# Optimization experiments

Hardware: AMD Instinct MI355X
Metric: run time of the kernel (lower is better)

## Reference

```python
import jax, jax.numpy as jnp
import numpy as np

B, T, N, E = 4, 30, 2000, 32000
F_IN, F_HID, F_GRU, N_CLS = 8, 64, 128, 2


def setup_inputs() -> dict:
    key = jax.random.key(0)
    ks = jax.random.split(key, 12)
    return {
        "x": jax.random.normal(ks[0], (B, T, N, F_IN), jnp.float32),
        "edge_index": jax.random.randint(ks[1], (B, T, 2, E), 0, N, jnp.int32),
        "W1": jax.random.normal(ks[2], (F_IN, F_HID), jnp.float32) * 0.1,
        "b1": jax.random.normal(ks[3], (F_HID,), jnp.float32) * 0.1,
        "W2": jax.random.normal(ks[4], (F_HID, F_HID), jnp.float32) * 0.1,
        "b2": jax.random.normal(ks[5], (F_HID,), jnp.float32) * 0.1,
        "W_ih": jax.random.normal(ks[6], (3 * F_GRU, F_HID), jnp.float32) * 0.1,
        "W_hh": jax.random.normal(ks[7], (3 * F_GRU, F_GRU), jnp.float32) * 0.1,
        "b_ih": jax.random.normal(ks[8], (3 * F_GRU,), jnp.float32) * 0.1,
        "b_hh": jax.random.normal(ks[9], (3 * F_GRU,), jnp.float32) * 0.1,
        "fc_w": jax.random.normal(ks[10], (N_CLS, F_GRU), jnp.float32) * 0.1,
        "fc_b": jax.random.normal(ks[11], (N_CLS,), jnp.float32) * 0.1,
    }


def _gcn_conv(x, src, dst, W, b):
    # PyG GCNConv (edge_weight=None): add self-loops, sym-normalize, x@W, scatter-add, +bias
    n = x.shape[0]
    loops = jnp.arange(n, dtype=src.dtype)
    s = jnp.concatenate([src, loops])
    d = jnp.concatenate([dst, loops])
    deg = jax.ops.segment_sum(jnp.ones(s.shape[0], x.dtype), d, num_segments=n)
    dis = jnp.where(deg > 0, jax.lax.rsqrt(deg), 0.0)
    norm = dis[s] * dis[d]                      # [E+N]
    h = x @ W                                   # [N, Fout]
    msg = h[s] * norm[:, None]                  # gather + scale
    return jax.ops.segment_sum(msg, d, num_segments=n) + b


def _frame_embed(x, ei, W1, b1, W2, b2):
    # one graph frame -> mean-pooled 64-d embedding
    src, dst = ei[0], ei[1]
    h = jax.nn.relu(_gcn_conv(x, src, dst, W1, b1))
    h = jax.nn.relu(_gcn_conv(h, src, dst, W2, b2))
    return h.mean(axis=0)


def _gru(H, W_ih, W_hh, b_ih, b_hh):
    # H: [T, B, F_HID]; torch GRU gate order: r, z, n
    def step(h, x_t):
        gi = x_t @ W_ih.T + b_ih                # [B, 3H]
        gh = h @ W_hh.T + b_hh
        i_r, i_z, i_n = jnp.split(gi, 3, axis=-1)
        h_r, h_z, h_n = jnp.split(gh, 3, axis=-1)
        r = jax.nn.sigmoid(i_r + h_r)
        z = jax.nn.sigmoid(i_z + h_z)
        n = jnp.tanh(i_n + r * h_n)
        h_new = (1.0 - z) * n + z * h
        return h_new, None
    h0 = jnp.zeros((H.shape[1], F_GRU), H.dtype)
    h_final, _ = jax.lax.scan(step, h0, H)
    return h_final                              # [B, F_GRU]


def reference(x, edge_index, W1, b1, W2, b2, W_ih, W_hh, b_ih, b_hh, fc_w, fc_b):
    G = B * T
    xf = x.reshape(G, N, F_IN)
    eif = edge_index.reshape(G, 2, E)
    emb = jax.vmap(_frame_embed, in_axes=(0, 0, None, None, None, None))(
        xf, eif, W1, b1, W2, b2)                # [G, 64]
    H = emb.reshape(B, T, F_HID).transpose(1, 0, 2)  # [T, B, 64]
    h_final = _gru(H, W_ih, W_hh, b_ih, b_hh)   # [B, 128]
    return h_final @ fc_w.T + fc_b              # [B, 2]
```

## Files before the change

kernel.cpp:

```cpp
#include <hip/hip_runtime.h>
#include <math.h>

#define G    120
#define Nn   2000
#define Ee   32000
#define Tt   30
#define Bb   4
#define Fg   128
#define QCAP 9216
#define TSLOT 48

static __device__ __forceinline__ unsigned short f2bf(float f) {
    unsigned u = __float_as_uint(f);
    u += 0x7fffu + ((u >> 16) & 1u);
    return (unsigned short)(u >> 16);
}

#if defined(__has_builtin)
#if __has_builtin(__builtin_amdgcn_cvt_f32_fp8) && __has_builtin(__builtin_amdgcn_cvt_pk_fp8_f32)
#define HW_FP8 1
#endif
#if __has_builtin(__builtin_amdgcn_cvt_pk_f32_fp8)
#define HW_FP8_PK 1
typedef float floatx2 __attribute__((ext_vector_type(2)));
#endif
#endif

static __device__ __forceinline__ unsigned fp8_enc_sw(float x) {
    unsigned s = (__float_as_uint(x) >> 24) & 0x80u;
    float ax = fminf(fabsf(x), 448.f);
    unsigned em;
    if (ax < 0.015625f) {
        em = (unsigned)__float2int_rn(ax * 512.f);
    } else {
        int e = (int)(__float_as_uint(ax) >> 23) - 127;
        float r = ax * __uint_as_float((unsigned)((130 - e) << 23));
        int q = __float2int_rn(r);
        em = (unsigned)(((e + 7) << 3) + (q - 8));
        em = min(em, 126u);
    }
    return s | em;
}
static __device__ __forceinline__ float fp8_dec_sw(unsigned b) {
    unsigned em = b & 0x7fu;
    float mag;
    if (em < 8u) mag = (float)em * 0.001953125f;
    else mag = __uint_as_float((((em >> 3) + 120u) << 23) | ((em & 7u) << 20));
    return (b & 0x80u) ? -mag : mag;
}
static __device__ __forceinline__ unsigned fp8_pack4(float a, float b, float c, float d) {
#ifdef HW_FP8
    int w = __builtin_amdgcn_cvt_pk_fp8_f32(a, b, 0, false);
    w = __builtin_amdgcn_cvt_pk_fp8_f32(c, d, w, true);
    return (unsigned)w;
#else
    return fp8_enc_sw(a) | (fp8_enc_sw(b) << 8) | (fp8_enc_sw(c) << 16) | (fp8_enc_sw(d) << 24);
#endif
}
static __device__ __forceinline__ void fp8x4_dec(unsigned dw, float* o) {
#ifdef HW_FP8_PK
    floatx2 lo = __builtin_amdgcn_cvt_pk_f32_fp8((int)dw, false);
    floatx2 hi = __builtin_amdgcn_cvt_pk_f32_fp8((int)dw, true);
    o[0] = lo[0]; o[1] = lo[1]; o[2] = hi[0]; o[3] = hi[1];
#else
    o[0] = fp8_dec_sw(dw & 0xffu);
    o[1] = fp8_dec_sw((dw >> 8) & 0xffu);
    o[2] = fp8_dec_sw((dw >> 16) & 0xffu);
    o[3] = fp8_dec_sw((dw >> 24) & 0xffu);
#endif
}

__global__ void __launch_bounds__(1024, 1)
k_build(const int* __restrict__ ei, float* __restrict__ dis,
        int* __restrict__ startA, int* __restrict__ csr,
        unsigned* __restrict__ ellT, int* __restrict__ cntS,
        int* __restrict__ ordS, float* __restrict__ emb) {
    __shared__ int   csr_l[Ee];
    __shared__ int   hist[Nn];
    __shared__ int   cntL[Nn];
    __shared__ int   nodeAt[Nn];
    __shared__ float disl[Nn];
    __shared__ int   dh[64];
    __shared__ int   db[64];
    __shared__ int   ovfS;
    int g = blockIdx.x;
    int tid = threadIdx.x;
    for (int idx = tid; idx < Nn; idx += 1024) hist[idx] = 0;
    if (tid < 64) dh[tid] = 0;
    if (tid == 0) ovfS = 0;
    if (tid < 64) emb[g * 64 + tid] = 0.f;
    __syncthreads();
    const int* srcp = ei + (size_t)g * 2 * Ee;
    const int* dstp = srcp + Ee;
    for (int it = tid; it < Ee / 4; it += 1024) {
        int4 d = reinterpret_cast<const int4*>(dstp)[it];
        atomicAdd(&hist[d.x], 1);
        atomicAdd(&hist[d.y], 1);
        atomicAdd(&hist[d.z], 1);
        atomicAdd(&hist[d.w], 1);
    }
    __syncthreads();
    for (int idx = tid; idx < Nn; idx += 1024) {
        int c = hist[idx];
        cntL[idx] = c;
        float dv = rsqrtf((float)c + 1.0f);
        disl[idx] = dv;
        dis[(size_t)g * Nn + idx] = dv;
        atomicAdd(&dh[min(c, 63)], 1);
        if (c > TSLOT - 1) atomicMax(&ovfS, 1);
    }
    __syncthreads();
    for (int off = 1; off < Nn; off <<= 1) {
        int i1 = tid + 1024;
        int v0 = (tid >= off) ? hist[tid - off] : 0;
        int v1 = (i1 < Nn && i1 >= off) ? hist[i1 - off] : 0;
        __syncthreads();
        hist[tid] += v0;
        if (i1 < Nn) hist[i1] += v1;
        __syncthreads();
    }
    if (tid == 0) {
        int s = 0;
        for (int b = 0; b < 64; ++b) { db[b] = s; s += dh[b]; }
    }
    __syncthreads();
    if (tid < 64) dh[tid] = db[tid];
    __syncthreads();
    for (int idx = tid; idx < Nn; idx += 1024) {
        int p = atomicAdd(&dh[min(cntL[idx], 63)], 1);
        nodeAt[p] = idx;
        hist[idx] -= cntL[idx];
    }
    __syncthreads();
    for (int it = tid; it < Ee / 4; it += 1024) {
        int4 d = reinterpret_cast<const int4*>(dstp)[it];
        int4 s = reinterpret_cast<const int4*>(srcp)[it];
        csr_l[atomicAdd(&hist[d.x], 1)] = s.x;
        csr_l[atomicAdd(&hist[d.y], 1)] = s.y;
        csr_l[atomicAdd(&hist[d.z], 1)] = s.z;
        csr_l[atomicAdd(&hist[d.w], 1)] = s.w;
    }
    __syncthreads();
    for (int c = tid; c < Nn; c += 1024) {
        int n2 = nodeAt[c];
        int cnt2 = cntL[n2];
        int ex2 = hist[n2] - cnt2;
        size_t gc = (size_t)g * Nn + c;
        cntS[gc] = cnt2;
        ordS[gc] = n2;
        startA[(size_t)g * Nn + n2] = g * 4 * QCAP + ex2;
        float dn2 = disl[n2];
        unsigned* et = ellT + (size_t)g * TSLOT * Nn + c;
        et[0] = (unsigned)n2 | ((unsigned)f2bf(dn2 * dn2) << 16);
        int m2 = min(cnt2, TSLOT - 1);
        for (int e = 0; e < m2; ++e) {
            int s = csr_l[ex2 + e];
            et[(size_t)(e + 1) * Nn] = (unsigned)s | ((unsigned)f2bf(disl[s] * dn2) << 16);
        }
    }
    __syncthreads();
    if (ovfS) {
        int* cg = csr + (size_t)g * 4 * QCAP;
        for (int it = tid; it < Ee; it += 1024) cg[it] = csr_l[it];
    }
}

__global__ void __launch_bounds__(256)
k_fused(const float* __restrict__ x, const unsigned* __restrict__ ellT,
        const int* __restrict__ cntS, const int* __restrict__ ordS,
        const int* __restrict__ startA, const int* __restrict__ csr,
        const float* __restrict__ dis,
        const float* __restrict__ W1, const float* __restrict__ b1,
        const float* __restrict__ W2, unsigned char* __restrict__ t2f) {
    int i = blockIdx.x;
    int xcd = i & 7;
    int j = i >> 3;
    int g = xcd * 15 + (j >> 3);
    int blk = j & 7;
    int p = blk * 256 + threadIdx.x;
    bool valid = (p < Nn);
    size_t gp = (size_t)g * Nn + (valid ? p : 0);
    int n = valid ? ordS[gp] : 0;
    int cnt = valid ? cntS[gp] : 0;
    int myc = valid ? (min(cnt, TSLOT - 1) + 1) : 0;
    float aX[8];
#pragma unroll
    for (int k = 0; k < 8; ++k) aX[k] = 0.f;
    {
        const unsigned* et = ellT + (size_t)g * TSLOT * Nn + (valid ? p : 0);
        const float4* x4 = reinterpret_cast<const float4*>(x + (size_t)g * Nn * 8);
        for (int e0 = 0; e0 < TSLOT; e0 += 8) {
            if (!__any(e0 < myc)) break;
            unsigned ub[8];
#pragma unroll
            for (int k = 0; k < 8; ++k)
                ub[k] = (e0 + k < myc) ? et[(size_t)(e0 + k) * Nn] : 0u;
#pragma unroll
            for (int k = 0; k < 8; ++k) {
                if (e0 + k < myc) {
                    float w = __uint_as_float(ub[k] & 0xffff0000u);
                    int s = ub[k] & 0xffffu;
                    float4 r0 = x4[s * 2], r1 = x4[s * 2 + 1];
                    aX[0] += r0.x * w; aX[1] += r0.y * w; aX[2] += r0.z * w; aX[3] += r0.w * w;
                    aX[4] += r1.x * w; aX[5] += r1.y * w; aX[6] += r1.z * w; aX[7] += r1.w * w;
                }
            }
        }
        if (cnt > TSLOT - 1) {
            size_t gn = (size_t)g * Nn + n;
            float dn = dis[gn];
            int start = startA[gn];
            const float* dsg = dis + (size_t)g * Nn;
            for (int e = TSLOT - 1; e < cnt; ++e) {
                int s = csr[start + e];
                float w = dsg[s] * dn;
                float4 r0 = x4[s * 2], r1 = x4[s * 2 + 1];
                aX[0] += r0.x * w; aX[1] += r0.y * w; aX[2] += r0.z * w; aX[3] += r0.w * w;
                aX[4] += r1.x * w; aX[5] += r1.y * w; aX[6] += r1.z * w; aX[7] += r1.w * w;
            }
        }
    }
    float h1r[64];
    {
        const float4* b14 = reinterpret_cast<const float4*>(b1);
#pragma unroll
        for (int f4 = 0; f4 < 16; ++f4) {
            float4 b = b14[f4];
            h1r[4 * f4 + 0] = b.x; h1r[4 * f4 + 1] = b.y;
            h1r[4 * f4 + 2] = b.z; h1r[4 * f4 + 3] = b.w;
        }
        const float4* W14 = reinterpret_cast<const float4*>(W1);
#pragma unroll
        for (int k = 0; k < 8; ++k) {
            float hk = aX[k];
#pragma unroll
            for (int f4 = 0; f4 < 16; ++f4) {
                float4 w = W14[k * 16 + f4];
                h1r[4 * f4 + 0] += hk * w.x; h1r[4 * f4 + 1] += hk * w.y;
                h1r[4 * f4 + 2] += hk * w.z; h1r[4 * f4 + 3] += hk * w.w;
            }
        }
#pragma unroll
        for (int f = 0; f < 64; ++f) h1r[f] = fmaxf(h1r[f], 0.f);
    }
    uint4 oh[2][2];
    {
        const float4* W24 = reinterpret_cast<const float4*>(W2);
#pragma unroll
        for (int hf = 0; hf < 2; ++hf) {
            float acch[32];
#pragma unroll
            for (int f = 0; f < 32; ++f) acch[f] = 0.f;
#pragma unroll
            for (int k = 0; k < 64; ++k) {
                float hk = h1r[k];
#pragma unroll
                for (int f4 = 0; f4 < 8; ++f4) {
                    float4 w = W24[k * 16 + hf * 8 + f4];
                    acch[4 * f4 + 0] += hk * w.x; acch[4 * f4 + 1] += hk * w.y;
                    acch[4 * f4 + 2] += hk * w.z; acch[4 * f4 + 3] += hk * w.w;
                }
            }
            oh[hf][0].x = fp8_pack4(acch[0],  acch[1],  acch[2],  acch[3]);
            oh[hf][0].y = fp8_pack4(acch[4],  acch[5],  acch[6],  acch[7]);
            oh[hf][0].z = fp8_pack4(acch[8],  acch[9],  acch[10], acch[11]);
            oh[hf][0].w = fp8_pack4(acch[12], acch[13], acch[14], acch[15]);
            oh[hf][1].x = fp8_pack4(acch[16], acch[17], acch[18], acch[19]);
            oh[hf][1].y = fp8_pack4(acch[20], acch[21], acch[22], acch[23]);
            oh[hf][1].z = fp8_pack4(acch[24], acch[25], acch[26], acch[27]);
            oh[hf][1].w = fp8_pack4(acch[28], acch[29], acch[30], acch[31]);
        }
    }
    if (valid) {
        uint4* op = reinterpret_cast<uint4*>(t2f + ((size_t)g * Nn + n) * 64);
        op[0] = oh[0][0]; op[1] = oh[0][1]; op[2] = oh[1][0]; op[3] = oh[1][1];
    }
}

__global__ void __launch_bounds__(1024, 1)
k_aggF(const unsigned char* __restrict__ t2f, const unsigned* __restrict__ ellT,
       const int* __restrict__ cntS, const int* __restrict__ ordS,
       const int* __restrict__ startA, const int* __restrict__ csr,
       const float* __restrict__ dis, const float* __restrict__ bias,
       float* __restrict__ emb) {
    __shared__ uint4 stage[Nn * 5];
    int i = blockIdx.x;
    int xcd = i & 7;
    int j = i >> 3;
    int g = xcd * 15 + (j >> 1);
    int half = j & 1;
    int tid = threadIdx.x;
    int w = tid >> 6, lane = tid & 63;
    {
        const uint4* src = reinterpret_cast<const uint4*>(t2f + (size_t)g * Nn * 64);
        for (int it = tid; it < Nn * 4; it += 1024)
            stage[(it >> 2) * 5 + (it & 3)] = src[it];
    }
    __syncthreads();
#define ROWFMA(dw, base) { float o_[4]; fp8x4_dec(dw, o_); \
    acc[base + 0] += o_[0] * wt; acc[base + 1] += o_[1] * wt; \
    acc[base + 2] += o_[2] * wt; acc[base + 3] += o_[3] * wt; }
#define EDGEFMA(s, wt) { \
    uint4 r0 = stage[(s) * 5], r1 = stage[(s) * 5 + 1]; \
    uint4 r2 = stage[(s) * 5 + 2], r3 = stage[(s) * 5 + 3]; \
    ROWFMA(r0.x, 0)  ROWFMA(r0.y, 4)  ROWFMA(r0.z, 8)  ROWFMA(r0.w, 12) \
    ROWFMA(r1.x, 16) ROWFMA(r1.y, 20) ROWFMA(r1.z, 24) ROWFMA(r1.w, 28) \
    ROWFMA(r2.x, 32) ROWFMA(r2.y, 36) ROWFMA(r2.z, 40) ROWFMA(r2.w, 44) \
    ROWFMA(r3.x, 48) ROWFMA(r3.y, 52) ROWFMA(r3.z, 56) ROWFMA(r3.w, 60) }
    int po = w * 64 + lane;
    int p = half * 1000 + po;
    bool valid = (po < 1000);
    size_t gp = (size_t)g * Nn + (valid ? p : 0);
    int cnt = valid ? cntS[gp] : 0;
    int myc = valid ? (min(cnt, TSLOT - 1) + 1) : 0;
    float acc[64];
#pragma unroll
    for (int k = 0; k < 64; ++k) acc[k] = 0.f;
    const unsigned* et = ellT + (size_t)g * TSLOT * Nn + (valid ? p : 0);
    unsigned u_cur = (0 < myc) ? et[0] : 0u;
    for (int e = 0; e < TSLOT; ++e) {
        if (!__any(e < myc)) break;
        unsigned u_nxt = ((e + 1) < TSLOT && (e + 1) < myc)
                             ? et[(size_t)(e + 1) * Nn] : 0u;
        if (e < myc) {
            float wt = __uint_as_float(u_cur & 0xffff0000u);
            int s = u_cur & 0xffffu;
            EDGEFMA(s, wt)
        }
        u_cur = u_nxt;
    }
    if (cnt > TSLOT - 1) {
        int n = ordS[gp];
        size_t gn = (size_t)g * Nn + n;
        float dn = dis[gn];
        int start = startA[gn];
        const float* dsg = dis + (size_t)g * Nn;
        for (int e = TSLOT - 1; e < cnt; ++e) {
            int s = csr[start + e];
            float wt = dsg[s] * dn;
            EDGEFMA(s, wt)
        }
    }
#undef EDGEFMA
#undef ROWFMA
    float pool = 0.f;
#pragma unroll
    for (int k = 0; k < 64; ++k) {
        float v = valid ? fmaxf(acc[k] + bias[k], 0.f) : 0.f;
        v += __shfl_xor(v, 1);  v += __shfl_xor(v, 2);  v += __shfl_xor(v, 4);
        v += __shfl_xor(v, 8);  v += __shfl_xor(v, 16); v += __shfl_xor(v, 32);
        if (lane == k) pool = v;
    }
    atomicAdd(&emb[g * 64 + lane], pool * (1.0f / Nn));
}

__global__ void __launch_bounds__(768, 1)
k_gru_seq(const float* __restrict__ emb, const float* __restrict__ W_ih,
          const float* __restrict__ b_ih, const float* __restrict__ W_hh,
          const float* __restrict__ b_hh, const float* __restrict__ fc_w,
          const float* __restrict__ fc_b, float* __restrict__ out) {
    __shared__ float h[Fg];
    __shared__ float part[768];
    __shared__ float embs[Tt][64];
    __shared__ float pgi[Tt][768];
    int b = blockIdx.x;
    int tid = threadIdx.x;
    int row = tid >> 1;
    int half = tid & 1;
    float w[64];
    const float* wr = W_hh + (size_t)row * Fg + half * 64;
#pragma unroll
    for (int i = 0; i < 64; ++i) w[i] = wr[i];
    float wih[32];
    const float* wir = W_ih + (size_t)row * 64 + half * 32;
#pragma unroll
    for (int i = 0; i < 32; ++i) wih[i] = wir[i];
    for (int it = tid; it < Tt * 64; it += 768)
        embs[it >> 6][it & 63] = emb[((size_t)b * Tt) * 64 + it];
    if (tid < Fg) h[tid] = 0.f;
    __syncthreads();
    for (int t = 0; t < Tt; ++t) {
        const float* e = &embs[t][half * 32];
        float a0 = 0.f, a1 = 0.f, a2 = 0.f, a3 = 0.f;
#pragma unroll
        for (int i = 0; i < 8; ++i) {
            a0 += wih[4 * i + 0] * e[4 * i + 0];
            a1 += wih[4 * i + 1] * e[4 * i + 1];
            a2 += wih[4 * i + 2] * e[4 * i + 2];
            a3 += wih[4 * i + 3] * e[4 * i + 3];
        }
        pgi[t][tid] = (a0 + a1) + (a2 + a3);
    }
    __syncthreads();
    for (int t = 0; t < Tt; ++t) {
        const float* hh = &h[half * 64];
        float a0 = 0.f, a1 = 0.f, a2 = 0.f, a3 = 0.f;
#pragma unroll
        for (int i = 0; i < 16; ++i) {
            a0 += w[4 * i + 0] * hh[4 * i + 0];
            a1 += w[4 * i + 1] * hh[4 * i + 1];
            a2 += w[4 * i + 2] * hh[4 * i + 2];
            a3 += w[4 * i + 3] * hh[4 * i + 3];
        }
        part[tid] = (a0 + a1) + (a2 + a3);
        __syncthreads();
        if (tid < Fg) {
            int j = tid;
            float hr = b_hh[j]       + part[2 * j]           + part[2 * j + 1];
            float hz = b_hh[128 + j] + part[2 * (128 + j)]   + part[2 * (128 + j) + 1];
            float hn = b_hh[256 + j] + part[2 * (256 + j)]   + part[2 * (256 + j) + 1];
            float gr = b_ih[j]       + pgi[t][2 * j]         + pgi[t][2 * j + 1];
            float gz = b_ih[128 + j] + pgi[t][2 * (128 + j)] + pgi[t][2 * (128 + j) + 1];
            float gn = b_ih[256 + j] + pgi[t][2 * (256 + j)] + pgi[t][2 * (256 + j) + 1];
            float r  = 1.f / (1.f + expf(-(gr + hr)));
            float z  = 1.f / (1.f + expf(-(gz + hz)));
            float nn = tanhf(gn + r * hn);
            h[j] = (1.f - z) * nn + z * h[j];
        }
        __syncthreads();
    }
    if (tid < 2) {
        float acc = fc_b[tid];
        for (int k = 0; k < Fg; ++k) acc += fc_w[tid * Fg + k] * h[k];
        out[b * 2 + tid] = acc;
    }
}

extern "C" void kernel_launch(void* const* d_in, const int* in_sizes, int n_in,
                              void* d_out, int out_size, void* d_ws, size_t ws_size,
                              hipStream_t stream) {
    const float* x     = (const float*)d_in[0];
    const int*   ei    = (const int*)  d_in[1];
    const float* W1    = (const float*)d_in[2];
    const float* b1    = (const float*)d_in[3];
    const float* W2    = (const float*)d_in[4];
    const float* b2    = (const float*)d_in[5];
    const float* W_ih  = (const float*)d_in[6];
    const float* W_hh  = (const float*)d_in[7];
    const float* b_ih  = (const float*)d_in[8];
    const float* b_hh  = (const float*)d_in[9];
    const float* fc_w  = (const float*)d_in[10];
    const float* fc_b  = (const float*)d_in[11];
    float* out = (float*)d_out;

    char* ws = (char*)d_ws;
    size_t off = 0;
    auto alloc = [&](size_t bytes) -> void* {
        void* p = ws + off;
        off = (off + bytes + 255) & ~(size_t)255;
        return p;
    };
    float*    dis    = (float*)   alloc((size_t)G * Nn * 4);
    int*      startA = (int*)     alloc((size_t)G * Nn * 4);
    int*      cntS   = (int*)     alloc((size_t)G * Nn * 4);
    int*      ordS   = (int*)     alloc((size_t)G * Nn * 4);
    int*      csr    = (int*)     alloc((size_t)G * 4 * QCAP * 4);
    unsigned* ellT   = (unsigned*)alloc((size_t)G * TSLOT * Nn * 4);
    unsigned char* t2f = (unsigned char*)alloc((size_t)G * Nn * 64);
    float*    emb    = (float*)   alloc((size_t)G * 64 * 4);
    (void)ws_size; (void)in_sizes; (void)n_in; (void)out_size;

    hipLaunchKernelGGL(k_build,   dim3(G), dim3(1024), 0, stream, ei, dis, startA, csr, ellT, cntS, ordS, emb);
    hipLaunchKernelGGL(k_fused,   dim3(960), dim3(256), 0, stream, x, ellT, cntS, ordS, startA, csr, dis, W1, b1, W2, t2f);
    hipLaunchKernelGGL(k_aggF,    dim3(240), dim3(1024), 0, stream, t2f, ellT, cntS, ordS, startA, csr, dis, b2, emb);
    hipLaunchKernelGGL(k_gru_seq, dim3(Bb), dim3(768), 0, stream, emb, W_ih, b_ih, W_hh, b_hh, fc_w, fc_b, out);
}
```

Baseline: 266.0 us.

## Fuse CSR build with first GCN layer, splitting each graph across two blocks

Merges the graph-build kernel and the first-layer aggregation/MLP kernel into one kernel. Each graph is processed by two 1024-thread blocks that both rebuild the shared-memory CSR redundantly, then each handles half the nodes, aggregating x straight from the LDS CSR and LDS degree table instead of re-reading the ELL table from global memory. This removes a kernel launch and the global round trip for the first layer, at the cost of duplicating the histogram and CSR construction work per graph. Emb zeroing and dis writes happen in both halves, and large LDS use keeps occupancy at one block per CU.

```diff
diff --git a/kernel.cpp b/kernel.cpp
--- a/kernel.cpp
+++ b/kernel.cpp
@@ -71,10 +71,12 @@
 }
 
 __global__ void __launch_bounds__(1024, 1)
-k_build(const int* __restrict__ ei, float* __restrict__ dis,
-        int* __restrict__ startA, int* __restrict__ csr,
-        unsigned* __restrict__ ellT, int* __restrict__ cntS,
-        int* __restrict__ ordS, float* __restrict__ emb) {
+k_bfuse(const int* __restrict__ ei, const float* __restrict__ x,
+        const float* __restrict__ W1, const float* __restrict__ b1,
+        const float* __restrict__ W2,
+        float* __restrict__ dis, int* __restrict__ startA, int* __restrict__ csr,
+        unsigned* __restrict__ ellT, int* __restrict__ cntS, int* __restrict__ ordS,
+        float* __restrict__ emb, unsigned char* __restrict__ t2f) {
     __shared__ int   csr_l[Ee];
     __shared__ int   hist[Nn];
     __shared__ int   cntL[Nn];
@@ -83,7 +85,9 @@
     __shared__ int   dh[64];
     __shared__ int   db[64];
     __shared__ int   ovfS;
-    int g = blockIdx.x;
+    int i = blockIdx.x;
+    int g = i >> 1;
+    int half = i & 1;
     int tid = threadIdx.x;
     for (int idx = tid; idx < Nn; idx += 1024) hist[idx] = 0;
     if (tid < 64) dh[tid] = 0;
@@ -141,7 +145,8 @@
         csr_l[atomicAdd(&hist[d.w], 1)] = s.w;
     }
     __syncthreads();
-    for (int c = tid; c < Nn; c += 1024) {
+    if (tid < 1000) {
+        int c = half * 1000 + tid;
         int n2 = nodeAt[c];
         int cnt2 = cntL[n2];
         int ex2 = hist[n2] - cnt2;
@@ -158,120 +163,92 @@
             et[(size_t)(e + 1) * Nn] = (unsigned)s | ((unsigned)f2bf(disl[s] * dn2) << 16);
         }
     }
-    __syncthreads();
-    if (ovfS) {
+    if (ovfS && half == 0) {
         int* cg = csr + (size_t)g * 4 * QCAP;
         for (int it = tid; it < Ee; it += 1024) cg[it] = csr_l[it];
     }
-}
-
-__global__ void __launch_bounds__(256)
-k_fused(const float* __restrict__ x, const unsigned* __restrict__ ellT,
-        const int* __restrict__ cntS, const int* __restrict__ ordS,
-        const int* __restrict__ startA, const int* __restrict__ csr,
-        const float* __restrict__ dis,
-        const float* __restrict__ W1, const float* __restrict__ b1,
-        const float* __restrict__ W2, unsigned char* __restrict__ t2f) {
-    int i = blockIdx.x;
-    int xcd = i & 7;
-    int j = i >> 3;
-    int g = xcd * 15 + (j >> 3);
-    int blk = j & 7;
-    int p = blk * 256 + threadIdx.x;
-    bool valid = (p < Nn);
-    size_t gp = (size_t)g * Nn + (valid ? p : 0);
-    int n = valid ? ordS[gp] : 0;
-    int cnt = valid ? cntS[gp] : 0;
-    int myc = valid ? (min(cnt, TSLOT - 1) + 1) : 0;
-    float aX[8];
-#pragma unroll
-    for (int k = 0; k < 8; ++k) aX[k] = 0.f;
-    {
-        const unsigned* et = ellT + (size_t)g * TSLOT * Nn + (valid ? p : 0);
+    __syncthreads();
+    if (tid < 1000) {
+        int c = half * 1000 + tid;
+        int n = nodeAt[c];
+        int cntn = cntL[n];
+        int ex = hist[n] - cntn;
+        float dn = disl[n];
         const float4* x4 = reinterpret_cast<const float4*>(x + (size_t)g * Nn * 8);
-        for (int e0 = 0; e0 < TSLOT; e0 += 8) {
-            if (!__any(e0 < myc)) break;
-            unsigned ub[8];
-#pragma unroll
-            for (int k = 0; k < 8; ++k)
-                ub[k] = (e0 + k < myc) ? et[(size_t)(e0 + k) * Nn] : 0u;
-#pragma unroll
-            for (int k = 0; k < 8; ++k) {
-                if (e0 + k < myc) {
-                    float w = __uint_as_float(ub[k] & 0xffff0000u);
-                    int s = ub[k] & 0xffffu;
+        float aX[8];
+        {
+            float w = dn * dn;
+            float4 r0 = x4[n * 2], r1 = x4[n * 2 + 1];
+            aX[0] = r0.x * w; aX[1] = r0.y * w; aX[2] = r0.z * w; aX[3] = r0.w * w;
+            aX[4] = r1.x * w; aX[5] = r1.y * w; aX[6] = r1.z * w; aX[7] = r1.w * w;
+        }
+        for (int e0 = 0; e0 < cntn; e0 += 8) {
+            int sb[8];
+#pragma unroll
+            for (int k2 = 0; k2 < 8; ++k2)
+                sb[k2] = (e0 + k2 < cntn) ? csr_l[ex + e0 + k2] : -1;
+#pragma unroll
+            for (int k2 = 0; k2 < 8; ++k2) {
+                if (sb[k2] >= 0) {
+                    int s = sb[k2];
+                    float w = disl[s] * dn;
                     float4 r0 = x4[s * 2], r1 = x4[s * 2 + 1];
                     aX[0] += r0.x * w; aX[1] += r0.y * w; aX[2] += r0.z * w; aX[3] += r0.w * w;
                     aX[4] += r1.x * w; aX[5] += r1.y * w; aX[6] += r1.z * w; aX[7] += r1.w * w;
                 }
             }
         }
-        if (cnt > TSLOT - 1) {
-            size_t gn = (size_t)g * Nn + n;
-            float dn = dis[gn];
-            int start = startA[gn];
-            const float* dsg = dis + (size_t)g * Nn;
-            for (int e = TSLOT - 1; e < cnt; ++e) {
-                int s = csr[start + e];
-                float w = dsg[s] * dn;
-                float4 r0 = x4[s * 2], r1 = x4[s * 2 + 1];
-                aX[0] += r0.x * w; aX[1] += r0.y * w; aX[2] += r0.z * w; aX[3] += r0.w * w;
-                aX[4] += r1.x * w; aX[5] += r1.y * w; aX[6] += r1.z * w; aX[7] += r1.w * w;
+        float h1r[64];
+        {
+            const float4* b14 = reinterpret_cast<const float4*>(b1);
+#pragma unroll
+            for (int f4 = 0; f4 < 16; ++f4) {
+                float4 b = b14[f4];
+                h1r[4 * f4 + 0] = b.x; h1r[4 * f4 + 1] = b.y;
+                h1r[4 * f4 + 2] = b.z; h1r[4 * f4 + 3] = b.w;
             }
-        }
-    }
-    float h1r[64];
-    {
-        const float4* b14 = reinterpret_cast<const float4*>(b1);
-#pragma unroll
-        for (int f4 = 0; f4 < 16; ++f4) {
-            float4 b = b14[f4];
-            h1r[4 * f4 + 0] = b.x; h1r[4 * f4 + 1] = b.y;
-            h1r[4 * f4 + 2] = b.z; h1r[4 * f4 + 3] = b.w;
-        }
-        const float4* W14 = reinterpret_cast<const float4*>(W1);
-#pragma unroll
-        for (int k = 0; k < 8; ++k) {
-            float hk = aX[k];
-#pragma unroll
-            for (int f4 = 0; f4 < 16; ++f4) {
-                float4 w = W14[k * 16 + f4];
-                h1r[4 * f4 + 0] += hk * w.x; h1r[4 * f4 + 1] += hk * w.y;
-                h1r[4 * f4 + 2] += hk * w.z; h1r[4 * f4 + 3] += hk * w.w;
-            }
-        }
-#pragma unroll
-        for (int f = 0; f < 64; ++f) h1r[f] = fmaxf(h1r[f], 0.f);
-    }
-    uint4 oh[2][2];
-    {
-        const float4* W24 = reinterpret_cast<const float4*>(W2);
-#pragma unroll
-        for (int hf = 0; hf < 2; ++hf) {
-            float acch[32];
-#pragma unroll
-            for (int f = 0; f < 32; ++f) acch[f] = 0.f;
-#pragma unroll
-            for (int k = 0; k < 64; ++k) {
-                float hk = h1r[k];
-#pragma unroll
-                for (int f4 = 0; f4 < 8; ++f4) {
-                    float4 w = W24[k * 16 + hf * 8 + f4];
-                    acch[4 * f4 + 0] += hk * w.x; acch[4 * f4 + 1] += hk * w.y;
-                    acch[4 * f4 + 2] += hk * w.z; acch[4 * f4 + 3] += hk * w.w;
+            const float4* W14 = reinterpret_cast<const float4*>(W1);
+#pragma unroll
+            for (int k2 = 0; k2 < 8; ++k2) {
+                float hk = aX[k2];
+#pragma unroll
+                for (int f4 = 0; f4 < 16; ++f4) {
+                    float4 w = W14[k2 * 16 + f4];
+                    h1r[4 * f4 + 0] += hk * w.x; h1r[4 * f4 + 1] += hk * w.y;
+                    h1r[4 * f4 + 2] += hk * w.z; h1r[4 * f4 + 3] += hk * w.w;
                 }
             }
-            oh[hf][0].x = fp8_pack4(acch[0],  acch[1],  acch[2],  acch[3]);
-            oh[hf][0].y = fp8_pack4(acch[4],  acch[5],  acch[6],  acch[7]);
-            oh[hf][0].z = fp8_pack4(acch[8],  acch[9],  acch[10], acch[11]);
-            oh[hf][0].w = fp8_pack4(acch[12], acch[13], acch[14], acch[15]);
-            oh[hf][1].x = fp8_pack4(acch[16], acch[17], acch[18], acch[19]);
-            oh[hf][1].y = fp8_pack4(acch[20], acch[21], acch[22], acch[23]);
-            oh[hf][1].z = fp8_pack4(acch[24], acch[25], acch[26], acch[27]);
-            oh[hf][1].w = fp8_pack4(acch[28], acch[29], acch[30], acch[31]);
-        }
-    }
-    if (valid) {
+#pragma unroll
+            for (int f = 0; f < 64; ++f) h1r[f] = fmaxf(h1r[f], 0.f);
+        }
+        uint4 oh[2][2];
+        {
+            const float4* W24 = reinterpret_cast<const float4*>(W2);
+#pragma unroll
+            for (int hf = 0; hf < 2; ++hf) {
+                float acch[32];
+#pragma unroll
+                for (int f = 0; f < 32; ++f) acch[f] = 0.f;
+#pragma unroll
+                for (int k2 = 0; k2 < 64; ++k2) {
+                    float hk = h1r[k2];
+#pragma unroll
+                    for (int f4 = 0; f4 < 8; ++f4) {
+                        float4 w = W24[k2 * 16 + hf * 8 + f4];
+                        acch[4 * f4 + 0] += hk * w.x; acch[4 * f4 + 1] += hk * w.y;
+                        acch[4 * f4 + 2] += hk * w.z; acch[4 * f4 + 3] += hk * w.w;
+                    }
+                }
+                oh[hf][0].x = fp8_pack4(acch[0],  acch[1],  acch[2],  acch[3]);
+                oh[hf][0].y = fp8_pack4(acch[4],  acch[5],  acch[6],  acch[7]);
+                oh[hf][0].z = fp8_pack4(acch[8],  acch[9],  acch[10], acch[11]);
+                oh[hf][0].w = fp8_pack4(acch[12], acch[13], acch[14], acch[15]);
+                oh[hf][1].x = fp8_pack4(acch[16], acch[17], acch[18], acch[19]);
+                oh[hf][1].y = fp8_pack4(acch[20], acch[21], acch[22], acch[23]);
+                oh[hf][1].z = fp8_pack4(acch[24], acch[25], acch[26], acch[27]);
+                oh[hf][1].w = fp8_pack4(acch[28], acch[29], acch[30], acch[31]);
+            }
+        }
         uint4* op = reinterpret_cast<uint4*>(t2f + ((size_t)g * Nn + n) * 64);
         op[0] = oh[0][0]; op[1] = oh[0][1]; op[2] = oh[1][0]; op[3] = oh[1][1];
     }
@@ -460,8 +437,8 @@
     float*    emb    = (float*)   alloc((size_t)G * 64 * 4);
     (void)ws_size; (void)in_sizes; (void)n_in; (void)out_size;
 
-    hipLaunchKernelGGL(k_build,   dim3(G), dim3(1024), 0, stream, ei, dis, startA, csr, ellT, cntS, ordS, emb);
-    hipLaunchKernelGGL(k_fused,   dim3(960), dim3(256), 0, stream, x, ellT, cntS, ordS, startA, csr, dis, W1, b1, W2, t2f);
+    hipLaunchKernelGGL(k_bfuse,   dim3(2 * G), dim3(1024), 0, stream,
+                       ei, x, W1, b1, W2, dis, startA, csr, ellT, cntS, ordS, emb, t2f);
     hipLaunchKernelGGL(k_aggF,    dim3(240), dim3(1024), 0, stream, t2f, ellT, cntS, ordS, startA, csr, dis, b2, emb);
     hipLaunchKernelGGL(k_gru_seq, dim3(Bb), dim3(768), 0, stream, emb, W_ih, b_ih, W_hh, b_hh, fc_w, fc_b, out);
 }
```

Result: faster. 255.5 us (-4.0%).
